# Optimization experiments

Measured on AMD Instinct MI355X. Metric: run time of the kernel, lower is better.

Reference implementation:

```python
import jax, jax.numpy as jnp
import numpy as np

O_FEAT = 4096
I_FEAT = 4096
NNZ = int(0.05 * O_FEAT * I_FEAT)  # 838860, matches k = int(residual.numel()*ortho_ratio)


def setup_inputs() -> dict:
    key = jax.random.key(0)
    k_x, k_pk, k_sc, k_v, k_r, k_c = jax.random.split(key, 6)
    x = jax.random.normal(k_x, (2, 1024, I_FEAT), dtype=jnp.float32)
    # packed int4 weights: each byte holds two 4-bit codes (offset-by-8 signed int4)
    base_packed = jax.random.randint(k_pk, (O_FEAT, I_FEAT // 2), 0, 256).astype(jnp.uint8)
    # per-output-row scales (robust_max / 7), strictly positive
    scales = jax.random.uniform(k_sc, (O_FEAT,), minval=1e-4, maxval=2e-2, dtype=jnp.float32)
    # sparse residual correction in fp16 (CSR values; represented as COO triplets)
    ortho_vals = (jax.random.normal(k_v, (NNZ,), dtype=jnp.float32) * 1e-2).astype(jnp.float16)
    ortho_rows = jax.random.randint(k_r, (NNZ,), 0, O_FEAT, dtype=jnp.int32)
    ortho_cols = jax.random.randint(k_c, (NNZ,), 0, I_FEAT, dtype=jnp.int32)
    return {
        "x": x,
        "base_packed": base_packed,
        "scales": scales,
        "ortho_vals": ortho_vals,
        "ortho_rows": ortho_rows,
        "ortho_cols": ortho_cols,
        "alpha": 1.0,
    }


def _dequant_int4(base_packed, scales):
    # unpack: low nibble -> even columns, high nibble -> odd columns
    O, Ih = base_packed.shape
    low = (base_packed & jnp.uint8(0x0F)).astype(jnp.int32)
    high = (base_packed >> 4).astype(jnp.int32)
    q = jnp.stack([low, high], axis=-1).reshape(O, Ih * 2)  # interleaved [l0,h0,l1,h1,...]
    return (q - 8).astype(jnp.float32) * scales[:, None]


def reference(x, base_packed, scales, ortho_vals, ortho_rows, ortho_cols, alpha):
    O, I = base_packed.shape[0], base_packed.shape[1] * 2
    w_base = _dequant_int4(base_packed, scales)  # [O, I] f32
    # scatter sparse residual into dense weight (same math as CSR spmm residual)
    w_sparse = jnp.zeros((O, I), jnp.float32).at[ortho_rows, ortho_cols].add(
        ortho_vals.astype(jnp.float32))
    W = w_base + alpha * w_sparse
    out = jnp.einsum("bsi,oi->bso", x.astype(jnp.float32), W)
    return out.astype(x.dtype)
```

## Files before the change

kernel.cpp:

```cpp
#include <hip/hip_runtime.h>
#include <hip/hip_fp16.h>
#include <stdint.h>

#define O_FEAT 4096
#define I_FEAT 4096
#define M_DIM  2048
#define K_DIM  4096

typedef __attribute__((ext_vector_type(8))) short short8;
typedef __attribute__((ext_vector_type(2))) short short2v;
typedef __attribute__((ext_vector_type(4))) float floatx4;

#define AS1 __attribute__((address_space(1)))
#define AS3 __attribute__((address_space(3)))

__device__ __forceinline__ uint16_t f32_to_bf16(float f) {
    uint32_t u = __builtin_bit_cast(uint32_t, f);
    u = (u + 0x7FFFu + ((u >> 16) & 1u)) >> 16;
    return (uint16_t)u;
}
__device__ __forceinline__ float bf16_to_f32(uint16_t h) {
    uint32_t u = ((uint32_t)h) << 16;
    return __builtin_bit_cast(float, u);
}

__device__ __forceinline__ void load_lds16(const uint16_t* gptr, uint16_t* ldsptr) {
    __builtin_amdgcn_global_load_lds((const AS1 uint32_t*)gptr,
                                     (AS3 uint32_t*)ldsptr, 16, 0, 0);
}

__global__ __launch_bounds__(256) void dequant_kernel(
        const void*  __restrict__ packed,
        const float* __restrict__ scales,
        uint16_t*    __restrict__ W) {
    const int lane = threadIdx.x & 63;
    uint32_t probe = ((const uint32_t*)packed)[lane];
    const bool int32mode = (__ballot(probe >= 256u) == 0ull);

    int idx = blockIdx.x * 256 + threadIdx.x;
    float s = scales[idx >> 9];

    uint32_t bytes4;
    if (int32mode) {
        uint4 w = ((const uint4*)packed)[idx];
        bytes4 = (w.x & 0xFFu) | ((w.y & 0xFFu) << 8) |
                 ((w.z & 0xFFu) << 16) | ((w.w & 0xFFu) << 24);
    } else {
        bytes4 = ((const uint32_t*)packed)[idx];
    }

    uint16_t o[8];
#pragma unroll
    for (int b = 0; b < 4; ++b) {
        int byte = (bytes4 >> (8 * b)) & 0xFF;
        o[2 * b]     = f32_to_bf16((float)((byte & 0xF) - 8) * s);
        o[2 * b + 1] = f32_to_bf16((float)((byte >> 4) - 8) * s);
    }
    uint4 v;
    v.x = (uint32_t)o[0] | ((uint32_t)o[1] << 16);
    v.y = (uint32_t)o[2] | ((uint32_t)o[3] << 16);
    v.z = (uint32_t)o[4] | ((uint32_t)o[5] << 16);
    v.w = (uint32_t)o[6] | ((uint32_t)o[7] << 16);
    ((uint4*)W)[idx] = v;
}

#define SCATTER_BLOCKS 3328
__global__ __launch_bounds__(256) void scatter_xconv_kernel(
        const void*  __restrict__ vals,
        const int*   __restrict__ rows,
        const int*   __restrict__ cols,
        const float* __restrict__ alpha,
        const float* __restrict__ x,
        uint16_t*    __restrict__ W,
        uint16_t*    __restrict__ Xb,
        int nnz) {
    if (blockIdx.x < SCATTER_BLOCKS) {
        const int lane = threadIdx.x & 63;
        float p = fabsf(((const float*)vals)[lane]);
        int cnt = __popcll(__ballot(p > 1e-4f && p < 1.0f));
        const bool f32mode = (cnt >= 32);

        int i = blockIdx.x * 256 + threadIdx.x;
        if (i >= nnz) return;
        float v = f32mode ? ((const float*)vals)[i]
                          : __half2float(((const __half*)vals)[i]);
        v *= alpha[0];
        int r = rows[i], c = cols[i];
        size_t elem = (size_t)r * I_FEAT + c;

#if __has_builtin(__builtin_amdgcn_global_atomic_fadd_v2bf16)
        const bool hi = (elem & 1);
        short b = (short)f32_to_bf16(v);
        short2v val;
        val[0] = hi ? (short)0 : b;
        val[1] = hi ? b : (short)0;
        __builtin_amdgcn_global_atomic_fadd_v2bf16(
            (AS1 short2v*)(W + (elem & ~(size_t)1)), val);
#else
        uint32_t* word = (uint32_t*)W + (elem >> 1);
        bool hi = (c & 1);
        uint32_t old = *word, assumed;
        do {
            assumed = old;
            uint16_t cur = hi ? (uint16_t)(assumed >> 16) : (uint16_t)(assumed & 0xFFFF);
            uint16_t nw  = f32_to_bf16(bf16_to_f32(cur) + v);
            uint32_t neww = hi ? ((assumed & 0x0000FFFFu) | ((uint32_t)nw << 16))
                               : ((assumed & 0xFFFF0000u) | (uint32_t)nw);
            old = atomicCAS(word, assumed, neww);
        } while (old != assumed);
#endif
    } else {
        int idx = (blockIdx.x - SCATTER_BLOCKS) * 256 + threadIdx.x;
        float4 v0 = ((const float4*)x)[2 * idx];
        float4 v1 = ((const float4*)x)[2 * idx + 1];
        uint4 o;
        o.x = (uint32_t)f32_to_bf16(v0.x) | ((uint32_t)f32_to_bf16(v0.y) << 16);
        o.y = (uint32_t)f32_to_bf16(v0.z) | ((uint32_t)f32_to_bf16(v0.w) << 16);
        o.z = (uint32_t)f32_to_bf16(v1.x) | ((uint32_t)f32_to_bf16(v1.y) << 16);
        o.w = (uint32_t)f32_to_bf16(v1.z) | ((uint32_t)f32_to_bf16(v1.w) << 16);
        ((uint4*)Xb)[idx] = o;
    }
}

#define BM 128
#define BN 128
#define BK 64
#define NT (K_DIM / BK)
#define BUF_ELEMS 16384

#define MFMA16(d, a, b) d = __builtin_amdgcn_mfma_f32_16x16x32_bf16(a, b, d, 0, 0, 0)

__global__ __launch_bounds__(256, 2) void gemm_bt_kernel(
        const uint16_t* __restrict__ A,
        const uint16_t* __restrict__ B,
        float* __restrict__ C) {
    __shared__ uint16_t lds[2 * BUF_ELEMS];

    const int tid  = threadIdx.x;
    const int wave = tid >> 6;
    const int lane = tid & 63;
    const int wm   = wave >> 1;
    const int wn   = wave & 1;

    const int wgid = blockIdx.y * 32 + blockIdx.x;
    const int swz  = (wgid & 7) * 64 + (wgid >> 3);
    const int bm0  = (swz >> 5) * BM;
    const int bn0  = (swz & 31) * BN;

    const int sr   = lane >> 3;
    const int xcol = ((lane & 7) ^ sr) << 3;
    const uint16_t* gA = A + (size_t)(bm0 + wave * 32 + sr) * K_DIM + xcol;
    const uint16_t* gB = B + (size_t)(bn0 + wave * 32 + sr) * K_DIM + xcol;
    const int ldsA = (wave * 32) * 64;
    const int ldsB = 8192 + (wave * 32) * 64;

    const int fr  = lane & 15;
    const int ko  = (lane >> 4) << 3;
    const int sk0 = (ko)      ^ ((fr & 7) << 3);
    const int sk1 = (32 + ko) ^ ((fr & 7) << 3);
    const int raA = (wm * 64 + fr) * BK;
    const int raB = 8192 + (wn * 64 + fr) * BK;

    floatx4 acc[4][4];
#pragma unroll
    for (int i = 0; i < 4; ++i)
#pragma unroll
        for (int j = 0; j < 4; ++j) acc[i][j] = {0.f, 0.f, 0.f, 0.f};

#pragma unroll
    for (int c = 0; c < 4; ++c)
        load_lds16(gA + (size_t)(c * 8) * K_DIM, &lds[ldsA + c * 512]);
#pragma unroll
    for (int c = 0; c < 4; ++c)
        load_lds16(gB + (size_t)(c * 8) * K_DIM, &lds[ldsB + c * 512]);
    asm volatile("s_waitcnt vmcnt(0)" ::: "memory");
    __builtin_amdgcn_s_barrier();

    for (int t = 0; t < NT; ++t) {
        const int cb = (t & 1) * BUF_ELEMS;
        const int sb = cb ^ BUF_ELEMS;
        const bool pf = (t + 1 < NT);
        const size_t kofs = (size_t)(t + 1) * BK;

        short8 a00 = *(const short8*)&lds[cb + raA + sk0];
        short8 a01 = *(const short8*)&lds[cb + raA + sk1];
        short8 a10 = *(const short8*)&lds[cb + raA + 1024 + sk0];
        short8 a11 = *(const short8*)&lds[cb + raA + 1024 + sk1];
        short8 b00 = *(const short8*)&lds[cb + raB + sk0];
        short8 b01 = *(const short8*)&lds[cb + raB + sk1];
        short8 b10 = *(const short8*)&lds[cb + raB + 1024 + sk0];
        short8 b11 = *(const short8*)&lds[cb + raB + 1024 + sk1];
        if (pf) {
            load_lds16(gA + kofs,                     &lds[sb + ldsA]);
            load_lds16(gA + kofs + (size_t)8 * K_DIM, &lds[sb + ldsA + 512]);
            load_lds16(gA + kofs + (size_t)16 * K_DIM,&lds[sb + ldsA + 1024]);
        }
        __builtin_amdgcn_s_barrier();
        asm volatile("s_waitcnt lgkmcnt(0)");
        __builtin_amdgcn_s_setprio(1);
        MFMA16(acc[0][0], a00, b00); MFMA16(acc[0][0], a01, b01);
        MFMA16(acc[0][1], a00, b10); MFMA16(acc[0][1], a01, b11);
        MFMA16(acc[1][0], a10, b00); MFMA16(acc[1][0], a11, b01);
        MFMA16(acc[1][1], a10, b10); MFMA16(acc[1][1], a11, b11);
        __builtin_amdgcn_s_setprio(0);
        __builtin_amdgcn_s_barrier();

        short8 b20 = *(const short8*)&lds[cb + raB + 2048 + sk0];
        short8 b21 = *(const short8*)&lds[cb + raB + 2048 + sk1];
        short8 b30 = *(const short8*)&lds[cb + raB + 3072 + sk0];
        short8 b31 = *(const short8*)&lds[cb + raB + 3072 + sk1];
        if (pf) {
            load_lds16(gA + kofs + (size_t)24 * K_DIM,&lds[sb + ldsA + 1536]);
            load_lds16(gB + kofs,                     &lds[sb + ldsB]);
            load_lds16(gB + kofs + (size_t)8 * K_DIM, &lds[sb + ldsB + 512]);
        }
        __builtin_amdgcn_s_barrier();
        asm volatile("s_waitcnt lgkmcnt(0)");
        __builtin_amdgcn_s_setprio(1);
        MFMA16(acc[0][2], a00, b20); MFMA16(acc[0][2], a01, b21);
        MFMA16(acc[0][3], a00, b30); MFMA16(acc[0][3], a01, b31);
        MFMA16(acc[1][2], a10, b20); MFMA16(acc[1][2], a11, b21);
        MFMA16(acc[1][3], a10, b30); MFMA16(acc[1][3], a11, b31);
        __builtin_amdgcn_s_setprio(0);
        __builtin_amdgcn_s_barrier();

        short8 a20 = *(const short8*)&lds[cb + raA + 2048 + sk0];
        short8 a21 = *(const short8*)&lds[cb + raA + 2048 + sk1];
        short8 a30 = *(const short8*)&lds[cb + raA + 3072 + sk0];
        short8 a31 = *(const short8*)&lds[cb + raA + 3072 + sk1];
        if (pf) {
            load_lds16(gB + kofs + (size_t)16 * K_DIM,&lds[sb + ldsB + 1024]);
            load_lds16(gB + kofs + (size_t)24 * K_DIM,&lds[sb + ldsB + 1536]);
        }
        __builtin_amdgcn_s_barrier();
        asm volatile("s_waitcnt lgkmcnt(0)");
        __builtin_amdgcn_s_setprio(1);
        MFMA16(acc[2][2], a20, b20); MFMA16(acc[2][2], a21, b21);
        MFMA16(acc[2][3], a20, b30); MFMA16(acc[2][3], a21, b31);
        MFMA16(acc[3][2], a30, b20); MFMA16(acc[3][2], a31, b21);
        MFMA16(acc[3][3], a30, b30); MFMA16(acc[3][3], a31, b31);
        __builtin_amdgcn_s_setprio(0);
        __builtin_amdgcn_s_barrier();

        __builtin_amdgcn_s_setprio(1);
        MFMA16(acc[2][0], a20, b00); MFMA16(acc[2][0], a21, b01);
        MFMA16(acc[2][1], a20, b10); MFMA16(acc[2][1], a21, b11);
        MFMA16(acc[3][0], a30, b00); MFMA16(acc[3][0], a31, b01);
        MFMA16(acc[3][1], a30, b10); MFMA16(acc[3][1], a31, b11);
        __builtin_amdgcn_s_setprio(0);
        if (pf) {
            asm volatile("s_waitcnt vmcnt(0)" ::: "memory");
            __builtin_amdgcn_s_barrier();
        }
    }

    const int cn  = lane & 15;
    const int rb4 = (lane >> 4) * 4;
#pragma unroll
    for (int i = 0; i < 4; ++i)
#pragma unroll
        for (int j = 0; j < 4; ++j)
#pragma unroll
            for (int r = 0; r < 4; ++r) {
                const int row = bm0 + wm * 64 + i * 16 + rb4 + r;
                const int col = bn0 + wn * 64 + j * 16 + cn;
                C[(size_t)row * O_FEAT + col] = acc[i][j][r];
            }
}

extern "C" void kernel_launch(void* const* d_in, const int* in_sizes, int n_in,
                              void* d_out, int out_size, void* d_ws, size_t ws_size,
                              hipStream_t stream) {
    const float* x      = (const float*)d_in[0];
    const void*  packed = d_in[1];
    const float* scales = (const float*)d_in[2];
    const void*  vals   = d_in[3];
    const int*   rows   = (const int*)d_in[4];
    const int*   cols   = (const int*)d_in[5];
    const float* alpha  = (const float*)d_in[6];
    float*       out    = (float*)d_out;
    const int nnz = in_sizes[3];

    uint16_t* W  = (uint16_t*)d_ws;
    uint16_t* Xb = (uint16_t*)((char*)d_ws + (size_t)O_FEAT * I_FEAT * 2);

    dequant_kernel<<<8192, 256, 0, stream>>>(packed, scales, W);
    scatter_xconv_kernel<<<SCATTER_BLOCKS + 4096, 256, 0, stream>>>(
        vals, rows, cols, alpha, x, W, Xb, nnz);
    gemm_bt_kernel<<<dim3(32, 16), 256, 0, stream>>>(Xb, W, out);
}
```

Baseline: 227.0 us.

## Use 256x256 GEMM tiles with split-K of two and atomic accumulation

The GEMM moves from 128x128 tiles with 256 threads to 256x256 tiles with 512 threads (8 waves, each owning a 128x64 sub-tile). K is split in two halves, giving 256 workgroups, and partial results are combined with float atomicAdd into an output that the scatter/convert kernel now zeroes. Larger tiles raise operand reuse per LDS load and cut global traffic, but they use 128 KB of LDS and 128 accumulator registers per thread, which may limit occupancy. The output also gets zeroing traffic plus atomic read-modify-write stores.

```diff
diff --git a/kernel.cpp b/kernel.cpp
--- a/kernel.cpp
+++ b/kernel.cpp
@@ -65,7 +65,9 @@
 }
 
 #define SCATTER_BLOCKS 3328
-__global__ __launch_bounds__(256) void scatter_xconv_kernel(
+#define XCONV_END      7424
+#define K2_BLOCKS      15616
+__global__ __launch_bounds__(256) void scatter_xconv_zero_kernel(
         const void*  __restrict__ vals,
         const int*   __restrict__ rows,
         const int*   __restrict__ cols,
@@ -73,6 +75,7 @@
         const float* __restrict__ x,
         uint16_t*    __restrict__ W,
         uint16_t*    __restrict__ Xb,
+        float*       __restrict__ C,
         int nnz) {
     if (blockIdx.x < SCATTER_BLOCKS) {
         const int lane = threadIdx.x & 63;
@@ -109,7 +112,7 @@
             old = atomicCAS(word, assumed, neww);
         } while (old != assumed);
 #endif
-    } else {
+    } else if (blockIdx.x < XCONV_END) {
         int idx = (blockIdx.x - SCATTER_BLOCKS) * 256 + threadIdx.x;
         float4 v0 = ((const float4*)x)[2 * idx];
         float4 v1 = ((const float4*)x)[2 * idx + 1];
@@ -119,134 +122,159 @@
         o.z = (uint32_t)f32_to_bf16(v1.x) | ((uint32_t)f32_to_bf16(v1.y) << 16);
         o.w = (uint32_t)f32_to_bf16(v1.z) | ((uint32_t)f32_to_bf16(v1.w) << 16);
         ((uint4*)Xb)[idx] = o;
+    } else {
+        int zidx = (blockIdx.x - XCONV_END) * 256 + threadIdx.x;
+        ((uint4*)C)[zidx] = uint4{0u, 0u, 0u, 0u};
     }
 }
 
-#define BM 128
-#define BN 128
 #define BK 64
-#define NT (K_DIM / BK)
-#define BUF_ELEMS 16384
-
-#define MFMA16(d, a, b) d = __builtin_amdgcn_mfma_f32_16x16x32_bf16(a, b, d, 0, 0, 0)
-
-__global__ __launch_bounds__(256, 2) void gemm_bt_kernel(
+#define NT_BLK 32
+#define DBUF 32768
+
+#define MF(i, j, A_, B_) acc[i][j] = __builtin_amdgcn_mfma_f32_16x16x32_bf16(A_, B_, acc[i][j], 0, 0, 0)
+#define ROW4(i, A_, B0_, B1_, B2_, B3_) \
+    MF(i, 0, A_, B0_); MF(i, 1, A_, B1_); MF(i, 2, A_, B2_); MF(i, 3, A_, B3_)
+
+__global__ __launch_bounds__(512, 2) void gemm_bt_kernel(
         const uint16_t* __restrict__ A,
         const uint16_t* __restrict__ B,
         float* __restrict__ C) {
-    __shared__ uint16_t lds[2 * BUF_ELEMS];
+    __shared__ uint16_t lds[2 * DBUF];
 
     const int tid  = threadIdx.x;
     const int wave = tid >> 6;
     const int lane = tid & 63;
-    const int wm   = wave >> 1;
-    const int wn   = wave & 1;
-
-    const int wgid = blockIdx.y * 32 + blockIdx.x;
-    const int swz  = (wgid & 7) * 64 + (wgid >> 3);
-    const int bm0  = (swz >> 5) * BM;
-    const int bn0  = (swz & 31) * BN;
-
-    const int sr   = lane >> 3;
-    const int xcol = ((lane & 7) ^ sr) << 3;
-    const uint16_t* gA = A + (size_t)(bm0 + wave * 32 + sr) * K_DIM + xcol;
-    const uint16_t* gB = B + (size_t)(bn0 + wave * 32 + sr) * K_DIM + xcol;
-    const int ldsA = (wave * 32) * 64;
-    const int ldsB = 8192 + (wave * 32) * 64;
+    const int wm   = wave >> 2;
+    const int wn   = wave & 3;
+
+    const int wgid = blockIdx.x;
+    const int swz  = (wgid & 7) * 32 + (wgid >> 3);
+    const int tile = swz >> 1;
+    const int ks   = swz & 1;
+    const int bm0  = (tile >> 4) * 256;
+    const int bn0  = (tile & 15) * 256;
+    const int kb   = ks * 2048;
+
+    const int srow = wave * 8 + (lane >> 3);
+    const int xcol = ((lane & 7) ^ (lane >> 3)) << 3;
+    const uint16_t* gA = A + (size_t)(bm0 + srow) * K_DIM + kb + xcol;
+    const uint16_t* gB = B + (size_t)(bn0 + srow) * K_DIM + kb + xcol;
+    const int ldsw = wave * 512;
 
     const int fr  = lane & 15;
     const int ko  = (lane >> 4) << 3;
     const int sk0 = (ko)      ^ ((fr & 7) << 3);
     const int sk1 = (32 + ko) ^ ((fr & 7) << 3);
-    const int raA = (wm * 64 + fr) * BK;
-    const int raB = 8192 + (wn * 64 + fr) * BK;
-
-    floatx4 acc[4][4];
-#pragma unroll
-    for (int i = 0; i < 4; ++i)
+    const int ao0 = (wm * 128 +   0 + fr) * 64;
+    const int ao1 = (wm * 128 +  16 + fr) * 64;
+    const int ao2 = (wm * 128 +  32 + fr) * 64;
+    const int ao3 = (wm * 128 +  48 + fr) * 64;
+    const int ao4 = (wm * 128 +  64 + fr) * 64;
+    const int ao5 = (wm * 128 +  80 + fr) * 64;
+    const int ao6 = (wm * 128 +  96 + fr) * 64;
+    const int ao7 = (wm * 128 + 112 + fr) * 64;
+    const int bo0 = 16384 + (wn * 64 +  0 + fr) * 64;
+    const int bo1 = 16384 + (wn * 64 + 16 + fr) * 64;
+    const int bo2 = 16384 + (wn * 64 + 32 + fr) * 64;
+    const int bo3 = 16384 + (wn * 64 + 48 + fr) * 64;
+
+    floatx4 acc[8][4];
+#pragma unroll
+    for (int i = 0; i < 8; ++i)
 #pragma unroll
         for (int j = 0; j < 4; ++j) acc[i][j] = {0.f, 0.f, 0.f, 0.f};
 
 #pragma unroll
     for (int c = 0; c < 4; ++c)
-        load_lds16(gA + (size_t)(c * 8) * K_DIM, &lds[ldsA + c * 512]);
+        load_lds16(gA + (size_t)(c * 64) * K_DIM, &lds[c * 4096 + ldsw]);
 #pragma unroll
     for (int c = 0; c < 4; ++c)
-        load_lds16(gB + (size_t)(c * 8) * K_DIM, &lds[ldsB + c * 512]);
+        load_lds16(gB + (size_t)(c * 64) * K_DIM, &lds[16384 + c * 4096 + ldsw]);
     asm volatile("s_waitcnt vmcnt(0)" ::: "memory");
     __builtin_amdgcn_s_barrier();
 
-    for (int t = 0; t < NT; ++t) {
-        const int cb = (t & 1) * BUF_ELEMS;
-        const int sb = cb ^ BUF_ELEMS;
-        const bool pf = (t + 1 < NT);
-        const size_t kofs = (size_t)(t + 1) * BK;
-
-        short8 a00 = *(const short8*)&lds[cb + raA + sk0];
-        short8 a01 = *(const short8*)&lds[cb + raA + sk1];
-        short8 a10 = *(const short8*)&lds[cb + raA + 1024 + sk0];
-        short8 a11 = *(const short8*)&lds[cb + raA + 1024 + sk1];
-        short8 b00 = *(const short8*)&lds[cb + raB + sk0];
-        short8 b01 = *(const short8*)&lds[cb + raB + sk1];
-        short8 b10 = *(const short8*)&lds[cb + raB + 1024 + sk0];
-        short8 b11 = *(const short8*)&lds[cb + raB + 1024 + sk1];
+    for (int t = 0; t < NT_BLK; ++t) {
+        const int  cb = (t & 1) << 15;
+        const int  sb = cb ^ DBUF;
+        const bool pf = (t + 1 < NT_BLK);
+        const int  kt = (t + 1) * BK;
+
+        short8 a0 = *(const short8*)&lds[cb + ao0 + sk0];
+        short8 a1 = *(const short8*)&lds[cb + ao1 + sk0];
+        short8 a2 = *(const short8*)&lds[cb + ao2 + sk0];
+        short8 a3 = *(const short8*)&lds[cb + ao3 + sk0];
+        short8 b0 = *(const short8*)&lds[cb + bo0 + sk0];
+        short8 b1 = *(const short8*)&lds[cb + bo1 + sk0];
+        short8 b2 = *(const short8*)&lds[cb + bo2 + sk0];
+        short8 b3 = *(const short8*)&lds[cb + bo3 + sk0];
         if (pf) {
-            load_lds16(gA + kofs,                     &lds[sb + ldsA]);
-            load_lds16(gA + kofs + (size_t)8 * K_DIM, &lds[sb + ldsA + 512]);
-            load_lds16(gA + kofs + (size_t)16 * K_DIM,&lds[sb + ldsA + 1024]);
+            load_lds16(gA + kt,                        &lds[sb + ldsw]);
+            load_lds16(gA + kt + (size_t) 64 * K_DIM,  &lds[sb + 4096 + ldsw]);
+            load_lds16(gA + kt + (size_t)128 * K_DIM,  &lds[sb + 8192 + ldsw]);
         }
         __builtin_amdgcn_s_barrier();
         asm volatile("s_waitcnt lgkmcnt(0)");
         __builtin_amdgcn_s_setprio(1);
-        MFMA16(acc[0][0], a00, b00); MFMA16(acc[0][0], a01, b01);
-        MFMA16(acc[0][1], a00, b10); MFMA16(acc[0][1], a01, b11);
-        MFMA16(acc[1][0], a10, b00); MFMA16(acc[1][0], a11, b01);
-        MFMA16(acc[1][1], a10, b10); MFMA16(acc[1][1], a11, b11);
+        ROW4(0, a0, b0, b1, b2, b3);
+        ROW4(1, a1, b0, b1, b2, b3);
+        ROW4(2, a2, b0, b1, b2, b3);
+        ROW4(3, a3, b0, b1, b2, b3);
         __builtin_amdgcn_s_setprio(0);
         __builtin_amdgcn_s_barrier();
 
-        short8 b20 = *(const short8*)&lds[cb + raB + 2048 + sk0];
-        short8 b21 = *(const short8*)&lds[cb + raB + 2048 + sk1];
-        short8 b30 = *(const short8*)&lds[cb + raB + 3072 + sk0];
-        short8 b31 = *(const short8*)&lds[cb + raB + 3072 + sk1];
+        short8 c0 = *(const short8*)&lds[cb + ao0 + sk1];
+        short8 c1 = *(const short8*)&lds[cb + ao1 + sk1];
+        short8 c2 = *(const short8*)&lds[cb + ao2 + sk1];
+        short8 c3 = *(const short8*)&lds[cb + ao3 + sk1];
+        short8 d0 = *(const short8*)&lds[cb + bo0 + sk1];
+        short8 d1 = *(const short8*)&lds[cb + bo1 + sk1];
+        short8 d2 = *(const short8*)&lds[cb + bo2 + sk1];
+        short8 d3 = *(const short8*)&lds[cb + bo3 + sk1];
         if (pf) {
-            load_lds16(gA + kofs + (size_t)24 * K_DIM,&lds[sb + ldsA + 1536]);
-            load_lds16(gB + kofs,                     &lds[sb + ldsB]);
-            load_lds16(gB + kofs + (size_t)8 * K_DIM, &lds[sb + ldsB + 512]);
+            load_lds16(gA + kt + (size_t)192 * K_DIM,  &lds[sb + 12288 + ldsw]);
+            load_lds16(gB + kt,                        &lds[sb + 16384 + ldsw]);
+            load_lds16(gB + kt + (size_t) 64 * K_DIM,  &lds[sb + 20480 + ldsw]);
         }
         __builtin_amdgcn_s_barrier();
         asm volatile("s_waitcnt lgkmcnt(0)");
         __builtin_amdgcn_s_setprio(1);
-        MFMA16(acc[0][2], a00, b20); MFMA16(acc[0][2], a01, b21);
-        MFMA16(acc[0][3], a00, b30); MFMA16(acc[0][3], a01, b31);
-        MFMA16(acc[1][2], a10, b20); MFMA16(acc[1][2], a11, b21);
-        MFMA16(acc[1][3], a10, b30); MFMA16(acc[1][3], a11, b31);
+        ROW4(0, c0, d0, d1, d2, d3);
+        ROW4(1, c1, d0, d1, d2, d3);
+        ROW4(2, c2, d0, d1, d2, d3);
+        ROW4(3, c3, d0, d1, d2, d3);
         __builtin_amdgcn_s_setprio(0);
         __builtin_amdgcn_s_barrier();
 
-        short8 a20 = *(const short8*)&lds[cb + raA + 2048 + sk0];
-        short8 a21 = *(const short8*)&lds[cb + raA + 2048 + sk1];
-        short8 a30 = *(const short8*)&lds[cb + raA + 3072 + sk0];
-        short8 a31 = *(const short8*)&lds[cb + raA + 3072 + sk1];
+        short8 e0 = *(const short8*)&lds[cb + ao4 + sk0];
+        short8 e1 = *(const short8*)&lds[cb + ao5 + sk0];
+        short8 e2 = *(const short8*)&lds[cb + ao6 + sk0];
+        short8 e3 = *(const short8*)&lds[cb + ao7 + sk0];
         if (pf) {
-            load_lds16(gB + kofs + (size_t)16 * K_DIM,&lds[sb + ldsB + 1024]);
-            load_lds16(gB + kofs + (size_t)24 * K_DIM,&lds[sb + ldsB + 1536]);
+            load_lds16(gB + kt + (size_t)128 * K_DIM,  &lds[sb + 24576 + ldsw]);
+            load_lds16(gB + kt + (size_t)192 * K_DIM,  &lds[sb + 28672 + ldsw]);
         }
         __builtin_amdgcn_s_barrier();
         asm volatile("s_waitcnt lgkmcnt(0)");
         __builtin_amdgcn_s_setprio(1);
-        MFMA16(acc[2][2], a20, b20); MFMA16(acc[2][2], a21, b21);
-        MFMA16(acc[2][3], a20, b30); MFMA16(acc[2][3], a21, b31);
-        MFMA16(acc[3][2], a30, b20); MFMA16(acc[3][2], a31, b21);
-        MFMA16(acc[3][3], a30, b30); MFMA16(acc[3][3], a31, b31);
+        ROW4(4, e0, b0, b1, b2, b3);
+        ROW4(5, e1, b0, b1, b2, b3);
+        ROW4(6, e2, b0, b1, b2, b3);
+        ROW4(7, e3, b0, b1, b2, b3);
         __builtin_amdgcn_s_setprio(0);
         __builtin_amdgcn_s_barrier();
 
+        short8 f0 = *(const short8*)&lds[cb + ao4 + sk1];
+        short8 f1 = *(const short8*)&lds[cb + ao5 + sk1];
+        short8 f2 = *(const short8*)&lds[cb + ao6 + sk1];
+        short8 f3 = *(const short8*)&lds[cb + ao7 + sk1];
+        __builtin_amdgcn_s_barrier();
+        asm volatile("s_waitcnt lgkmcnt(0)");
         __builtin_amdgcn_s_setprio(1);
-        MFMA16(acc[2][0], a20, b00); MFMA16(acc[2][0], a21, b01);
-        MFMA16(acc[2][1], a20, b10); MFMA16(acc[2][1], a21, b11);
-        MFMA16(acc[3][0], a30, b00); MFMA16(acc[3][0], a31, b01);
-        MFMA16(acc[3][1], a30, b10); MFMA16(acc[3][1], a31, b11);
+        ROW4(4, f0, d0, d1, d2, d3);
+        ROW4(5, f1, d0, d1, d2, d3);
+        ROW4(6, f2, d0, d1, d2, d3);
+        ROW4(7, f3, d0, d1, d2, d3);
         __builtin_amdgcn_s_setprio(0);
         if (pf) {
             asm volatile("s_waitcnt vmcnt(0)" ::: "memory");
@@ -257,14 +285,14 @@
     const int cn  = lane & 15;
     const int rb4 = (lane >> 4) * 4;
 #pragma unroll
-    for (int i = 0; i < 4; ++i)
+    for (int i = 0; i < 8; ++i)
 #pragma unroll
         for (int j = 0; j < 4; ++j)
 #pragma unroll
             for (int r = 0; r < 4; ++r) {
-                const int row = bm0 + wm * 64 + i * 16 + rb4 + r;
+                const int row = bm0 + wm * 128 + i * 16 + rb4 + r;
                 const int col = bn0 + wn * 64 + j * 16 + cn;
-                C[(size_t)row * O_FEAT + col] = acc[i][j][r];
+                atomicAdd(&C[(size_t)row * O_FEAT + col], acc[i][j][r]);
             }
 }
 
@@ -285,7 +313,7 @@
     uint16_t* Xb = (uint16_t*)((char*)d_ws + (size_t)O_FEAT * I_FEAT * 2);
 
     dequant_kernel<<<8192, 256, 0, stream>>>(packed, scales, W);
-    scatter_xconv_kernel<<<SCATTER_BLOCKS + 4096, 256, 0, stream>>>(
-        vals, rows, cols, alpha, x, W, Xb, nnz);
-    gemm_bt_kernel<<<dim3(32, 16), 256, 0, stream>>>(Xb, W, out);
-}
+    scatter_xconv_zero_kernel<<<K2_BLOCKS, 256, 0, stream>>>(
+        vals, rows, cols, alpha, x, W, Xb, out, nnz);
+    gemm_bt_kernel<<<256, 512, 0, stream>>>(Xb, W, out);
+}
```

Result: slower. 266.4 us (+17.3%).
